# Kernel tuning notes

Measured on AMD Instinct MI355X. Metric: run time of the kernel, lower is better.

The kernel has to match this reference:

```python
import jax, jax.numpy as jnp
import numpy as np

T, B, I, H = 4096, 2048, 1, 10


def setup_inputs() -> dict:
    key = jax.random.key(0)
    ks = jax.random.split(key, 8)
    k = 1.0 / np.sqrt(H)  # torch default init bound for RNN and Linear(10,1)
    u = lambda kk, shape: jax.random.uniform(kk, shape, jnp.float32, -k, k)
    return {
        "x": jax.random.normal(ks[0], (T, B, I), jnp.float32),
        "h": jnp.zeros((1, B, H), jnp.float32),
        "W_ih": u(ks[1], (H, I)),
        "b_ih": u(ks[2], (H,)),
        "W_hh": u(ks[3], (H, H)),
        "b_hh": u(ks[4], (H,)),
        "W_out": u(ks[5], (1, H)),
        "b_out": u(ks[6], (1,)),
    }


def reference(x, h, W_ih, b_ih, W_hh, b_hh, W_out, b_out):
    # Vanilla RNN: h_t = tanh(x_t @ W_ih^T + b_ih + h_{t-1} @ W_hh^T + b_hh)
    b = b_ih + b_hh  # fuse the two biases once

    def step(h_prev, x_t):  # h_prev: [B,H], x_t: [B,I]
        h_new = jnp.tanh(x_t @ W_ih.T + h_prev @ W_hh.T + b)
        return h_new, h_new

    h_last, ys = jax.lax.scan(step, h[0], x)  # ys: [T,B,H]
    out = ys @ W_out.T + b_out  # [T,B,1]
    return out, h_last[None]  # h: [1,B,H]
```

## Files before the change

### kernel.cpp

```cpp
#include <hip/hip_runtime.h>

#define T_STEPS 4096
#define BATCH   2048
#define HID     10
#define UB      16

__device__ __forceinline__ void issue16(float (&xr)[UB], const float* base) {
#pragma unroll
    for (int u = 0; u < UB; ++u)
        asm volatile("global_load_dword %0, %1, off"
                     : "=v"(xr[u]) : "v"(base + (size_t)u * BATCH) : "memory");
}
#define BIND16(a) "+v"(a[0]),"+v"(a[1]),"+v"(a[2]),"+v"(a[3]),"+v"(a[4]), \
    "+v"(a[5]),"+v"(a[6]),"+v"(a[7]),"+v"(a[8]),"+v"(a[9]),"+v"(a[10]),   \
    "+v"(a[11]),"+v"(a[12]),"+v"(a[13]),"+v"(a[14]),"+v"(a[15])
__device__ __forceinline__ void wait1_bind(float (&xr)[UB]) {
    asm volatile("s_waitcnt vmcnt(1)" : BIND16(xr) :: "memory");
}
__device__ __forceinline__ void wait0_bind(float (&xr)[UB]) {
    asm volatile("s_waitcnt vmcnt(0)" : BIND16(xr) :: "memory");
}

__device__ __forceinline__ void step_blob(float& r, float& p, float& pk,
                                          float x, float wih2, float bj2,
                                          float wo2, float m,
                                          const float (&w)[16]) {
    float c0, c1;
    asm volatile(
        "v_fma_f32 %[c0], %[wih2], %[x], %[bj2]\n\t"
        "v_mul_f32 %[p], %[wo2], %[r]\n\t"
        "v_mul_f32_dpp %[c1], %[r], %[w4] row_ror:4 row_mask:0xf bank_mask:0xf\n\t"
        "v_fmac_f32 %[c0], %[r], %[w0]\n\t"
        "v_fmac_f32_dpp %[c1], %[r], %[w5] row_ror:5 row_mask:0xf bank_mask:0xf\n\t"
        "v_add_f32_dpp %[p], %[p], %[p] row_ror:8 row_mask:0xf bank_mask:0xf\n\t"
        "v_fmac_f32_dpp %[c0], %[r], %[w1] row_ror:1 row_mask:0xf bank_mask:0xf\n\t"
        "v_fmac_f32_dpp %[c1], %[r], %[w6] row_ror:6 row_mask:0xf bank_mask:0xf\n\t"
        "v_add_f32_dpp %[p], %[p], %[p] row_ror:4 row_mask:0xf bank_mask:0xf\n\t"
        "v_fmac_f32_dpp %[c0], %[r], %[w2] row_ror:2 row_mask:0xf bank_mask:0xf\n\t"
        "v_fmac_f32_dpp %[c1], %[r], %[w7] row_ror:7 row_mask:0xf bank_mask:0xf\n\t"
        "v_add_f32_dpp %[p], %[p], %[p] row_ror:2 row_mask:0xf bank_mask:0xf\n\t"
        "v_fmac_f32_dpp %[c0], %[r], %[w3] row_ror:3 row_mask:0xf bank_mask:0xf\n\t"
        "v_fmac_f32_dpp %[c1], %[r], %[w8] row_ror:8 row_mask:0xf bank_mask:0xf\n\t"
        "v_add_f32_dpp %[p], %[p], %[p] row_ror:1 row_mask:0xf bank_mask:0xf\n\t"
        "v_fmac_f32_dpp %[c0], %[r], %[w10] row_ror:10 row_mask:0xf bank_mask:0xf\n\t"
        "v_fmac_f32_dpp %[c1], %[r], %[w9] row_ror:9 row_mask:0xf bank_mask:0xf\n\t"
        "v_fmac_f32 %[pk], %[p], %[m]\n\t"
        "v_fmac_f32_dpp %[c0], %[r], %[w12] row_ror:12 row_mask:0xf bank_mask:0xf\n\t"
        "v_fmac_f32_dpp %[c1], %[r], %[w11] row_ror:11 row_mask:0xf bank_mask:0xf\n\t"
        "v_fmac_f32_dpp %[c0], %[r], %[w14] row_ror:14 row_mask:0xf bank_mask:0xf\n\t"
        "v_fmac_f32_dpp %[c1], %[r], %[w13] row_ror:13 row_mask:0xf bank_mask:0xf\n\t"
        "v_fmac_f32_dpp %[c0], %[r], %[w15] row_ror:15 row_mask:0xf bank_mask:0xf\n\t"
        "v_add_f32 %[c0], %[c0], %[c1]\n\t"
        "v_exp_f32 %[c0], %[c0]\n\t"
        "s_nop 0\n\t"
        "v_add_f32 %[c0], 1.0, %[c0]\n\t"
        "v_rcp_f32 %[r], %[c0]\n\t"
        "s_nop 0"
        : [c0]"=&v"(c0), [c1]"=&v"(c1), [r]"+v"(r), [p]"+v"(p), [pk]"+v"(pk)
        : [x]"v"(x), [wih2]"v"(wih2), [bj2]"v"(bj2), [wo2]"v"(wo2), [m]"v"(m),
          [w0]"v"(w[0]),  [w1]"v"(w[1]),  [w2]"v"(w[2]),  [w3]"v"(w[3]),
          [w4]"v"(w[4]),  [w5]"v"(w[5]),  [w6]"v"(w[6]),  [w7]"v"(w[7]),
          [w8]"v"(w[8]),  [w9]"v"(w[9]),  [w10]"v"(w[10]),[w11]"v"(w[11]),
          [w12]"v"(w[12]),[w13]"v"(w[13]),[w14]"v"(w[14]),[w15]"v"(w[15]));
}

__device__ __forceinline__ void finish_reduce(float r, float& p, float& pk,
                                              float wo2, float m15) {
    asm volatile(
        "v_mul_f32 %[p], %[wo2], %[r]\n\t"
        "s_nop 1\n\t"
        "v_add_f32_dpp %[p], %[p], %[p] row_ror:8 row_mask:0xf bank_mask:0xf\n\t"
        "s_nop 1\n\t"
        "v_add_f32_dpp %[p], %[p], %[p] row_ror:4 row_mask:0xf bank_mask:0xf\n\t"
        "s_nop 1\n\t"
        "v_add_f32_dpp %[p], %[p], %[p] row_ror:2 row_mask:0xf bank_mask:0xf\n\t"
        "s_nop 1\n\t"
        "v_add_f32_dpp %[p], %[p], %[p] row_ror:1 row_mask:0xf bank_mask:0xf\n\t"
        "s_nop 1\n\t"
        "v_fmac_f32 %[pk], %[p], %[m]"
        : [p]"+v"(p), [pk]"+v"(pk)
        : [r]"v"(r), [wo2]"v"(wo2), [m]"v"(m15));
}

__global__ __launch_bounds__(64, 1) void rnn_kernel(
    const float* __restrict__ x,
    const float* __restrict__ h0,
    const float* __restrict__ W_ih,
    const float* __restrict__ b_ih,
    const float* __restrict__ W_hh,
    const float* __restrict__ b_hh,
    const float* __restrict__ W_out,
    const float* __restrict__ b_out,
    float* __restrict__ out)
{
    const int tid = threadIdx.x;
    const int j   = tid & 15;
    const int b   = (blockIdx.x << 2) + (tid >> 4);
    const bool jv = (j < HID);
    const int jc  = jv ? j : 0;

    const float CC = 2.88539008177792681472f;

    const float wih = jv ? W_ih[jc] : 0.0f;
    const float bj  = jv ? (b_ih[jc] + b_hh[jc]) : 0.0f;
    const float wo  = jv ? W_out[jc] : 0.0f;

    float wsh[16];
    float wsum = 0.0f;
#pragma unroll
    for (int N = 0; N < 16; ++N) {
        const int k = (j - N) & 15;
        wsh[N] = (jv && k < HID) ? W_hh[jc * HID + k] : 0.0f;
        wsum += wsh[N];
    }

    const float wih2 = CC * wih;
    const float bj2  = CC * (bj + wsum);
    float w2[16];
#pragma unroll
    for (int N = 0; N < 16; ++N) w2[N] = -2.0f * CC * wsh[N];
    const float wo2 = -2.0f * wo;
    float c0sum = b_out[0];
#pragma unroll
    for (int k = 0; k < HID; ++k) c0sum += W_out[k];

    float km[16];
#pragma unroll
    for (int i = 0; i < 16; ++i) km[i] = (j == i) ? 1.0f : 0.0f;
    const float mzero = 0.0f;

    float rval = fmaf(-0.5f, jv ? h0[b * HID + jc] : 0.0f, 0.5f);
    float p = 0.0f, pk = 0.0f;

    const float* xb = x + b;
    float xA[UB], xB[UB];

    issue16(xA, xb);
    wait0_bind(xA);

    for (int t0 = 0; t0 < T_STEPS; t0 += 2 * UB) {
        wait1_bind(xA);
        issue16(xB, xb + (size_t)(t0 + UB) * BATCH);
#pragma unroll
        for (int u = 0; u < UB; ++u)
            step_blob(rval, p, pk, xA[u], wih2, bj2, wo2,
                      (u == 0) ? mzero : km[u - 1], w2);
        finish_reduce(rval, p, pk, wo2, km[15]);
        out[(size_t)(t0 + j) * BATCH + b] = pk + c0sum;
        pk = 0.0f;

        wait1_bind(xB);
        const float* xsrc = (t0 + 2 * UB < T_STEPS)
                          ? (xb + (size_t)(t0 + 2 * UB) * BATCH) : xb;
        issue16(xA, xsrc);
#pragma unroll
        for (int u = 0; u < UB; ++u)
            step_blob(rval, p, pk, xB[u], wih2, bj2, wo2,
                      (u == 0) ? mzero : km[u - 1], w2);
        finish_reduce(rval, p, pk, wo2, km[15]);
        out[(size_t)(t0 + UB + j) * BATCH + b] = pk + c0sum;
        pk = 0.0f;
    }

    wait0_bind(xA);

    if (jv) out[(size_t)T_STEPS * BATCH + (size_t)b * HID + j]
                = fmaf(-2.0f, rval, 1.0f);
}

extern "C" void kernel_launch(void* const* d_in, const int* in_sizes, int n_in,
                              void* d_out, int out_size, void* d_ws, size_t ws_size,
                              hipStream_t stream) {
    const float* x     = (const float*)d_in[0];
    const float* h0    = (const float*)d_in[1];
    const float* W_ih  = (const float*)d_in[2];
    const float* b_ih  = (const float*)d_in[3];
    const float* W_hh  = (const float*)d_in[4];
    const float* b_hh  = (const float*)d_in[5];
    const float* W_out = (const float*)d_in[6];
    const float* b_out = (const float*)d_in[7];

    rnn_kernel<<<BATCH / 4, 64, 0, stream>>>(
        x, h0, W_ih, b_ih, W_hh, b_hh, W_out, b_out, (float*)d_out);
}
```

Before: 358.5 us.

## Fold output projection into spare lane 10 of the recurrent matvec

The separate per-step output reduction (a multiply plus four DPP adds) is removed. Lane 10, which was otherwise idle, now gets -2*W_out weights, so its pre-activation sum c0 equals the output projection of the previous hidden state. That value is picked up with a single rotated DPP fmac into pk, using a compile-time rotation chosen per unrolled step. The matvec is also split into three accumulator chains instead of two to shorten the dependency chain, at the cost of more variants of inline asm and tricky lane and rotation bookkeeping.

```diff
diff --git a/kernel.cpp b/kernel.cpp
--- a/kernel.cpp
+++ b/kernel.cpp
@@ -21,47 +21,101 @@
     asm volatile("s_waitcnt vmcnt(0)" : BIND16(xr) :: "memory");
 }
 
-__device__ __forceinline__ void step_blob(float& r, float& p, float& pk,
-                                          float x, float wih2, float bj2,
-                                          float wo2, float m,
-                                          const float (&w)[16]) {
-    float c0, c1;
-    asm volatile(
-        "v_fma_f32 %[c0], %[wih2], %[x], %[bj2]\n\t"
-        "v_mul_f32 %[p], %[wo2], %[r]\n\t"
-        "v_mul_f32_dpp %[c1], %[r], %[w4] row_ror:4 row_mask:0xf bank_mask:0xf\n\t"
-        "v_fmac_f32 %[c0], %[r], %[w0]\n\t"
-        "v_fmac_f32_dpp %[c1], %[r], %[w5] row_ror:5 row_mask:0xf bank_mask:0xf\n\t"
-        "v_add_f32_dpp %[p], %[p], %[p] row_ror:8 row_mask:0xf bank_mask:0xf\n\t"
-        "v_fmac_f32_dpp %[c0], %[r], %[w1] row_ror:1 row_mask:0xf bank_mask:0xf\n\t"
-        "v_fmac_f32_dpp %[c1], %[r], %[w6] row_ror:6 row_mask:0xf bank_mask:0xf\n\t"
-        "v_add_f32_dpp %[p], %[p], %[p] row_ror:4 row_mask:0xf bank_mask:0xf\n\t"
-        "v_fmac_f32_dpp %[c0], %[r], %[w2] row_ror:2 row_mask:0xf bank_mask:0xf\n\t"
-        "v_fmac_f32_dpp %[c1], %[r], %[w7] row_ror:7 row_mask:0xf bank_mask:0xf\n\t"
-        "v_add_f32_dpp %[p], %[p], %[p] row_ror:2 row_mask:0xf bank_mask:0xf\n\t"
-        "v_fmac_f32_dpp %[c0], %[r], %[w3] row_ror:3 row_mask:0xf bank_mask:0xf\n\t"
-        "v_fmac_f32_dpp %[c1], %[r], %[w8] row_ror:8 row_mask:0xf bank_mask:0xf\n\t"
-        "v_add_f32_dpp %[p], %[p], %[p] row_ror:1 row_mask:0xf bank_mask:0xf\n\t"
-        "v_fmac_f32_dpp %[c0], %[r], %[w10] row_ror:10 row_mask:0xf bank_mask:0xf\n\t"
-        "v_fmac_f32_dpp %[c1], %[r], %[w9] row_ror:9 row_mask:0xf bank_mask:0xf\n\t"
-        "v_fmac_f32 %[pk], %[p], %[m]\n\t"
-        "v_fmac_f32_dpp %[c0], %[r], %[w12] row_ror:12 row_mask:0xf bank_mask:0xf\n\t"
-        "v_fmac_f32_dpp %[c1], %[r], %[w11] row_ror:11 row_mask:0xf bank_mask:0xf\n\t"
-        "v_fmac_f32_dpp %[c0], %[r], %[w14] row_ror:14 row_mask:0xf bank_mask:0xf\n\t"
-        "v_fmac_f32_dpp %[c1], %[r], %[w13] row_ror:13 row_mask:0xf bank_mask:0xf\n\t"
-        "v_fmac_f32_dpp %[c0], %[r], %[w15] row_ror:15 row_mask:0xf bank_mask:0xf\n\t"
-        "v_add_f32 %[c0], %[c0], %[c1]\n\t"
-        "v_exp_f32 %[c0], %[c0]\n\t"
-        "s_nop 0\n\t"
-        "v_add_f32 %[c0], 1.0, %[c0]\n\t"
-        "v_rcp_f32 %[r], %[c0]\n\t"
-        "s_nop 0"
-        : [c0]"=&v"(c0), [c1]"=&v"(c1), [r]"+v"(r), [p]"+v"(p), [pk]"+v"(pk)
-        : [x]"v"(x), [wih2]"v"(wih2), [bj2]"v"(bj2), [wo2]"v"(wo2), [m]"v"(m),
-          [w0]"v"(w[0]),  [w1]"v"(w[1]),  [w2]"v"(w[2]),  [w3]"v"(w[3]),
-          [w4]"v"(w[4]),  [w5]"v"(w[5]),  [w6]"v"(w[6]),  [w7]"v"(w[7]),
-          [w8]"v"(w[8]),  [w9]"v"(w[9]),  [w10]"v"(w[10]),[w11]"v"(w[11]),
-          [w12]"v"(w[12]),[w13]"v"(w[13]),[w14]"v"(w[14]),[w15]"v"(w[15]));
+#define STEP_HEAD \
+    "v_fma_f32 %[c0], %[wih2], %[x], %[bj2]\n\t"                                    \
+    "v_fmac_f32 %[c0], %[r], %[w0]\n\t"                                             \
+    "v_mul_f32_dpp %[c1], %[r], %[w1] row_ror:1 row_mask:0xf bank_mask:0xf\n\t"     \
+    "v_mul_f32_dpp %[c2], %[r], %[w2] row_ror:2 row_mask:0xf bank_mask:0xf\n\t"     \
+    "v_fmac_f32_dpp %[c0], %[r], %[w3] row_ror:3 row_mask:0xf bank_mask:0xf\n\t"    \
+    "v_fmac_f32_dpp %[c1], %[r], %[w4] row_ror:4 row_mask:0xf bank_mask:0xf\n\t"    \
+    "v_fmac_f32_dpp %[c2], %[r], %[w5] row_ror:5 row_mask:0xf bank_mask:0xf\n\t"    \
+    "v_fmac_f32_dpp %[c0], %[r], %[w6] row_ror:6 row_mask:0xf bank_mask:0xf\n\t"    \
+    "v_fmac_f32_dpp %[c1], %[r], %[w7] row_ror:7 row_mask:0xf bank_mask:0xf\n\t"    \
+    "v_fmac_f32_dpp %[c2], %[r], %[w8] row_ror:8 row_mask:0xf bank_mask:0xf\n\t"    \
+    "v_fmac_f32_dpp %[c0], %[r], %[w9] row_ror:9 row_mask:0xf bank_mask:0xf\n\t"    \
+    "v_fmac_f32_dpp %[c1], %[r], %[w10] row_ror:10 row_mask:0xf bank_mask:0xf\n\t"  \
+    "v_fmac_f32_dpp %[c2], %[r], %[w11] row_ror:11 row_mask:0xf bank_mask:0xf\n\t"  \
+    "v_fmac_f32_dpp %[c0], %[r], %[w12] row_ror:12 row_mask:0xf bank_mask:0xf\n\t"  \
+    "v_fmac_f32_dpp %[c1], %[r], %[w13] row_ror:13 row_mask:0xf bank_mask:0xf\n\t"  \
+    "v_fmac_f32_dpp %[c2], %[r], %[w14] row_ror:14 row_mask:0xf bank_mask:0xf\n\t"  \
+    "v_fmac_f32_dpp %[c0], %[r], %[w15] row_ror:15 row_mask:0xf bank_mask:0xf\n\t"  \
+    "v_add_f32 %[c1], %[c1], %[c2]\n\t"                                             \
+    "v_add_f32 %[c0], %[c0], %[c1]\n\t"                                             \
+    "v_exp_f32 %[ex], %[c0]\n\t"                                                    \
+    "s_nop 0\n\t"                                                                   \
+    "v_add_f32 %[ex], 1.0, %[ex]\n\t"
+
+#define STEP_TAIL \
+    "v_rcp_f32 %[r], %[ex]\n\t"                                                     \
+    "s_nop 0"
+
+#define PKDPP(N) "v_fmac_f32_dpp %[pk], %[c0], %[m] row_ror:" #N " row_mask:0xf bank_mask:0xf\n\t"
+#define PKPLAIN  "v_fmac_f32 %[pk], %[c0], %[m]\n\t"
+
+#define DEF_STEP(SUF, PKLINE_) \
+__device__ __forceinline__ void step_##SUF(float& r, float& pk, float x, \
+        float wih2, float bj2, float m, const float (&w)[16]) { \
+    float c0, c1, c2, ex; \
+    asm volatile( STEP_HEAD PKLINE_ STEP_TAIL \
+        : [c0]"=&v"(c0), [c1]"=&v"(c1), [c2]"=&v"(c2), [ex]"=&v"(ex), \
+          [r]"+v"(r), [pk]"+v"(pk) \
+        : [x]"v"(x), [wih2]"v"(wih2), [bj2]"v"(bj2), [m]"v"(m), \
+          [w0]"v"(w[0]),  [w1]"v"(w[1]),  [w2]"v"(w[2]),  [w3]"v"(w[3]), \
+          [w4]"v"(w[4]),  [w5]"v"(w[5]),  [w6]"v"(w[6]),  [w7]"v"(w[7]), \
+          [w8]"v"(w[8]),  [w9]"v"(w[9]),  [w10]"v"(w[10]),[w11]"v"(w[11]), \
+          [w12]"v"(w[12]),[w13]"v"(w[13]),[w14]"v"(w[14]),[w15]"v"(w[15])); \
+}
+
+DEF_STEP(r0,  PKPLAIN)
+DEF_STEP(r1,  PKDPP(1))
+DEF_STEP(r2,  PKDPP(2))
+DEF_STEP(r3,  PKDPP(3))
+DEF_STEP(r4,  PKDPP(4))
+DEF_STEP(r6,  PKDPP(6))
+DEF_STEP(r7,  PKDPP(7))
+DEF_STEP(r8,  PKDPP(8))
+DEF_STEP(r9,  PKDPP(9))
+DEF_STEP(r10, PKDPP(10))
+DEF_STEP(r11, PKDPP(11))
+DEF_STEP(r12, PKDPP(12))
+DEF_STEP(r13, PKDPP(13))
+DEF_STEP(r14, PKDPP(14))
+DEF_STEP(r15, PKDPP(15))
+
+template<int U>
+__device__ __forceinline__ void step_u(float& r, float& pk, float x,
+                                       float wih2, float bj2,
+                                       const float (&km)[16], float mz,
+                                       const float (&w)[16]) {
+    constexpr int ROT = (U + 5) & 15;
+    float m;
+    if constexpr (U == 0) m = mz; else m = km[U - 1];
+    if constexpr (ROT == 0)       step_r0 (r, pk, x, wih2, bj2, m, w);
+    else if constexpr (ROT == 1)  step_r1 (r, pk, x, wih2, bj2, m, w);
+    else if constexpr (ROT == 2)  step_r2 (r, pk, x, wih2, bj2, m, w);
+    else if constexpr (ROT == 3)  step_r3 (r, pk, x, wih2, bj2, m, w);
+    else if constexpr (ROT == 4)  step_r4 (r, pk, x, wih2, bj2, m, w);
+    else if constexpr (ROT == 6)  step_r6 (r, pk, x, wih2, bj2, m, w);
+    else if constexpr (ROT == 7)  step_r7 (r, pk, x, wih2, bj2, m, w);
+    else if constexpr (ROT == 8)  step_r8 (r, pk, x, wih2, bj2, m, w);
+    else if constexpr (ROT == 9)  step_r9 (r, pk, x, wih2, bj2, m, w);
+    else if constexpr (ROT == 10) step_r10(r, pk, x, wih2, bj2, m, w);
+    else if constexpr (ROT == 11) step_r11(r, pk, x, wih2, bj2, m, w);
+    else if constexpr (ROT == 12) step_r12(r, pk, x, wih2, bj2, m, w);
+    else if constexpr (ROT == 13) step_r13(r, pk, x, wih2, bj2, m, w);
+    else if constexpr (ROT == 14) step_r14(r, pk, x, wih2, bj2, m, w);
+    else                          step_r15(r, pk, x, wih2, bj2, m, w);
+}
+
+template<int U>
+__device__ __forceinline__ void run16(float& r, float& pk, const float (&xr)[UB],
+                                      float wih2, float bj2,
+                                      const float (&km)[16], float mz,
+                                      const float (&w)[16]) {
+    if constexpr (U < UB) {
+        step_u<U>(r, pk, xr[U], wih2, bj2, km, mz, w);
+        run16<U + 1>(r, pk, xr, wih2, bj2, km, mz, w);
+    }
 }
 
 __device__ __forceinline__ void finish_reduce(float r, float& p, float& pk,
@@ -118,7 +172,16 @@
     const float bj2  = CC * (bj + wsum);
     float w2[16];
 #pragma unroll
-    for (int N = 0; N < 16; ++N) w2[N] = -2.0f * CC * wsh[N];
+    for (int N = 0; N < 16; ++N) {
+        if (jv) {
+            w2[N] = -2.0f * CC * wsh[N];
+        } else if (j == 10) {
+            const int k = (10 - N) & 15;
+            w2[N] = (k < HID) ? (-2.0f * W_out[k]) : 0.0f;
+        } else {
+            w2[N] = 0.0f;
+        }
+    }
     const float wo2 = -2.0f * wo;
     float c0sum = b_out[0];
 #pragma unroll
@@ -141,10 +204,7 @@
     for (int t0 = 0; t0 < T_STEPS; t0 += 2 * UB) {
         wait1_bind(xA);
         issue16(xB, xb + (size_t)(t0 + UB) * BATCH);
-#pragma unroll
-        for (int u = 0; u < UB; ++u)
-            step_blob(rval, p, pk, xA[u], wih2, bj2, wo2,
-                      (u == 0) ? mzero : km[u - 1], w2);
+        run16<0>(rval, pk, xA, wih2, bj2, km, mzero, w2);
         finish_reduce(rval, p, pk, wo2, km[15]);
         out[(size_t)(t0 + j) * BATCH + b] = pk + c0sum;
         pk = 0.0f;
@@ -153,10 +213,7 @@
         const float* xsrc = (t0 + 2 * UB < T_STEPS)
                           ? (xb + (size_t)(t0 + 2 * UB) * BATCH) : xb;
         issue16(xA, xsrc);
-#pragma unroll
-        for (int u = 0; u < UB; ++u)
-            step_blob(rval, p, pk, xB[u], wih2, bj2, wo2,
-                      (u == 0) ? mzero : km[u - 1], w2);
+        run16<0>(rval, pk, xB, wih2, bj2, km, mzero, w2);
         finish_reduce(rval, p, pk, wo2, km[15]);
         out[(size_t)(t0 + UB + j) * BATCH + b] = pk + c0sum;
         pk = 0.0f;
```

New measurement: 331.1 us. -7.7%, faster.
